# Performance work log

Measured on AMD Instinct MI355X. Metric: run time of the kernel, lower is better.

Reference implementation:

```python
import jax, jax.numpy as jnp
import numpy as np

N, E, B = 100000, 1000000, 64
DIN, DS, H, NG = 128, 1024, 256, 20


def setup_inputs() -> dict:
    key = jax.random.key(0)
    ks = jax.random.split(key, 48)
    lin = lambda k, i, o: (jax.random.normal(k, (i, o), jnp.float32) / np.sqrt(i)).astype(jnp.float32)
    inp = {
        'x': jax.random.normal(ks[0], (N, DIN), jnp.float32),
        'edge_index': jax.random.randint(ks[1], (2, E), 0, N, jnp.int32),
        'batch': jnp.sort(jax.random.randint(ks[2], (N,), 0, B, jnp.int32)),
        'static_features': jax.random.normal(ks[3], (B, DS), jnp.float32),
        'temporal_feats': jax.random.normal(ks[4], (B, 5), jnp.float32),
        'type_idx': jax.random.randint(ks[5], (B,), 0, 10, jnp.int32),
        'type_emb': jax.random.normal(ks[6], (10, H), jnp.float32),
        # static encoder
        'Ws1': lin(ks[7], DS, H), 'bs1': jnp.zeros(H), 'Ws2': lin(ks[8], H, H), 'bs2': jnp.zeros(H),
        # 3 GCN convs
        'Wc1': lin(ks[9], DIN, H), 'bc1': jnp.zeros(H),
        'Wc2': lin(ks[10], H, H), 'bc2': jnp.zeros(H),
        'Wc3': lin(ks[11], H, H), 'bc3': jnp.zeros(H),
        # residual dim_match linears
        'Wd1': lin(ks[12], DIN, H), 'bd1': jnp.zeros(H),
        'Wd2': lin(ks[13], H, H), 'bd2': jnp.zeros(H),
        'Wd3': lin(ks[14], H, H), 'bd3': jnp.zeros(H),
        # temporal MLP (5 -> H//2 -> H)
        'Wt1': lin(ks[15], 5, H // 2), 'bt1': jnp.zeros(H // 2),
        'Wt2': lin(ks[16], H // 2, H), 'bt2': jnp.zeros(H),
        # pattern detector
        'Wp1': lin(ks[17], H, H // 2), 'bp1': jnp.zeros(H // 2),
        'Wp2': lin(ks[18], H // 2, H), 'bp2': jnp.zeros(H),
        # fusion (5H -> 2H -> H)
        'Wf1': lin(ks[19], 5 * H, 2 * H), 'bf1': jnp.zeros(2 * H),
        'Wf2': lin(ks[20], 2 * H, H), 'bf2': jnp.zeros(H),
        # heads
        'Wg': lin(ks[21], H, NG), 'bg': jnp.zeros(NG),
        'Wtp': lin(ks[22], H, 1), 'btp': jnp.zeros(1),
    }
    return inp


def reference(x, edge_index, batch, static_features, temporal_feats, type_idx, type_emb,
              Ws1, bs1, Ws2, bs2,
              Wc1, bc1, Wc2, bc2, Wc3, bc3,
              Wd1, bd1, Wd2, bd2, Wd3, bd3,
              Wt1, bt1, Wt2, bt2,
              Wp1, bp1, Wp2, bp2,
              Wf1, bf1, Wf2, bf2,
              Wg, bg, Wtp, btp):
    n = x.shape[0]
    b = static_features.shape[0]
    src, dst = edge_index[0], edge_index[1]
    # GCN symmetric norm with self-loops: deg = 1 + in-degree
    deg = 1.0 + jax.ops.segment_sum(jnp.ones(src.shape[0], x.dtype), dst, num_segments=n)
    dinv = deg ** -0.5
    ew = dinv[src] * dinv[dst]  # [E] edge norm weights

    def gcn(h_in, W, bias):
        h = h_in @ W  # [n, H]
        agg = jax.ops.segment_sum(h[src] * ew[:, None], dst, num_segments=n)
        return agg + h / deg[:, None] + bias  # neighbor agg + self-loop + bias

    # 3 GCN layers with residual dim_match (dropout is identity at inference)
    x1 = jax.nn.relu(gcn(x, Wc1, bc1)) + (x @ Wd1 + bd1)
    x2 = jax.nn.relu(gcn(x1, Wc2, bc2)) + (x1 @ Wd2 + bd2)
    x3 = jax.nn.relu(gcn(x2, Wc3, bc3)) + (x2 @ Wd3 + bd3)

    pat = jax.nn.relu(jax.nn.relu(x3 @ Wp1 + bp1) @ Wp2 + bp2)

    counts = jnp.maximum(jax.ops.segment_sum(jnp.ones(n, x.dtype), batch, num_segments=b), 1.0)
    graph_embed = jax.ops.segment_sum(x3, batch, num_segments=b) / counts[:, None]
    pattern_embed = jax.ops.segment_sum(pat, batch, num_segments=b) / counts[:, None]

    static_embed = jax.nn.relu(static_features @ Ws1 + bs1) @ Ws2 + bs2
    temporal_embed = jax.nn.relu(temporal_feats @ Wt1 + bt1) @ Wt2 + bt2
    type_embed = type_emb[type_idx]

    combined = jnp.concatenate([graph_embed, static_embed, temporal_embed, type_embed, pattern_embed], axis=1)
    fused = jax.nn.relu(combined @ Wf1 + bf1) @ Wf2 + bf2
    group_logits = fused @ Wg + bg
    time_pred = fused @ Wtp + btp
    return fused, group_logits, time_pred
```

## Files before the change

### kernel.cpp

```cpp
#include <hip/hip_runtime.h>

#define H 256
#define LDK 40

typedef __attribute__((ext_vector_type(8))) short bf16x8;
typedef __attribute__((ext_vector_type(4))) float f32x4;

__device__ __forceinline__ float b2f(ushort h) {
    return __uint_as_float(((unsigned)h) << 16);
}
__device__ __forceinline__ float b2f_lo(unsigned u) {
    return __uint_as_float(u << 16);
}
__device__ __forceinline__ float b2f_hi(unsigned u) {
    return __uint_as_float(u & 0xffff0000u);
}
__device__ __forceinline__ ushort f2bf(float f) {
    unsigned u = __float_as_uint(f);
    unsigned r = (u + 0x7FFF + ((u >> 16) & 1)) >> 16;
    return (ushort)r;
}
__device__ __forceinline__ unsigned pack2bf(float lo, float hi) {
    return (unsigned)f2bf(lo) | ((unsigned)f2bf(hi) << 16);
}

__device__ __forceinline__ void gload16(const ushort* g, const short* l) {
    __builtin_amdgcn_global_load_lds(
        (const __attribute__((address_space(1))) void*)(const void*)g,
        (__attribute__((address_space(3))) void*)(void*)l, 16, 0, 0);
}

__global__ __launch_bounds__(256) void k_zero2_i(int* p, int* q, int n) {
    int i = blockIdx.x * 256 + threadIdx.x;
    if (i < n) { p[i] = 0; q[i] = 0; }
}

__global__ __launch_bounds__(256) void k_zero_f(float* p, int n) {
    int i = blockIdx.x * 256 + threadIdx.x;
    if (i < n) p[i] = 0.f;
}

__global__ __launch_bounds__(256) void k_count_deg_i(const int* __restrict__ dst, int* cnt, int E) {
    int i = blockIdx.x * 256 + threadIdx.x;
    if (i < E) atomicAdd(&cnt[dst[i]], 1);
}

__global__ __launch_bounds__(256) void k_scan1(const int* __restrict__ cnt, int* __restrict__ partial,
                                               int* __restrict__ bsums, int N) {
    __shared__ int s[256];
    int t = threadIdx.x;
    int idx = blockIdx.x * 256 + t;
    int v = idx < N ? cnt[idx] : 0;
    s[t] = v;
    __syncthreads();
    for (int off = 1; off < 256; off <<= 1) {
        int add = (t >= off) ? s[t - off] : 0;
        __syncthreads();
        s[t] += add;
        __syncthreads();
    }
    if (idx < N) partial[idx] = s[t];
    if (t == 255) bsums[blockIdx.x] = s[t];
}

__global__ __launch_bounds__(1024) void k_scan2(int* bsums, int nb) {
    __shared__ int s[1024];
    int t = threadIdx.x;
    s[t] = (t < nb) ? bsums[t] : 0;
    __syncthreads();
    for (int off = 1; off < 1024; off <<= 1) {
        int add = (t >= off) ? s[t - off] : 0;
        __syncthreads();
        s[t] += add;
        __syncthreads();
    }
    if (t < nb) bsums[t] = s[t];
}

__global__ __launch_bounds__(256) void k_scan3(const int* __restrict__ partial, const int* __restrict__ bsums,
                                               const int* __restrict__ cnt,
                                               int* __restrict__ rowptr, float* __restrict__ dinv,
                                               float* __restrict__ selfw, int N) {
    int idx = blockIdx.x * 256 + threadIdx.x;
    if (idx < N) {
        int off = blockIdx.x > 0 ? bsums[blockIdx.x - 1] : 0;
        rowptr[idx + 1] = partial[idx] + off;
        if (idx == 0) rowptr[0] = 0;
        float d = 1.0f + (float)cnt[idx];
        dinv[idx] = rsqrtf(d);
        selfw[idx] = 1.0f / d;
    }
}

__global__ __launch_bounds__(256) void k_scatter(const int* __restrict__ src, const int* __restrict__ dst,
                                                 const float* __restrict__ dinv, const int* __restrict__ rowptr,
                                                 int* __restrict__ fill, int* __restrict__ esrc,
                                                 float* __restrict__ ewt, int E) {
    int e = blockIdx.x * 256 + threadIdx.x;
    if (e >= E) return;
    int s = src[e], d = dst[e];
    int pos = rowptr[d] + atomicAdd(&fill[d], 1);
    esrc[pos] = s;
    ewt[pos] = dinv[s] * dinv[d];
}

__device__ __forceinline__ void tcvt_one(long i, const float* __restrict__ W, ushort* __restrict__ Wt,
                                         int K, int M) {
    int k = (int)(i / M), m = (int)(i - (long)k * M);
    Wt[(size_t)m * K + k] = f2bf(W[(size_t)k * M + m]);
}

__global__ __launch_bounds__(256) void k_prep(
    const float* __restrict__ x, ushort* __restrict__ xh, long nx, int DIN,
    const float* __restrict__ Wc1, ushort* Wc1t, const float* __restrict__ Wd1, ushort* Wd1t,
    const float* __restrict__ Wc2, ushort* Wc2t, const float* __restrict__ Wd2, ushort* Wd2t,
    const float* __restrict__ Wc3, ushort* Wc3t, const float* __restrict__ Wd3, ushort* Wd3t,
    const float* __restrict__ Wp1, ushort* Wp1t, const float* __restrict__ Wp2, ushort* Wp2t) {
    long i = (long)blockIdx.x * 256 + threadIdx.x;
    if (i < nx) { xh[i] = f2bf(x[i]); return; }
    i -= nx;
    long n1 = (long)DIN * 256;
    if (i < n1) { tcvt_one(i, Wc1, Wc1t, DIN, 256); return; }
    i -= n1;
    if (i < n1) { tcvt_one(i, Wd1, Wd1t, DIN, 256); return; }
    i -= n1;
    if (i < 65536) { tcvt_one(i, Wc2, Wc2t, 256, 256); return; }
    i -= 65536;
    if (i < 65536) { tcvt_one(i, Wd2, Wd2t, 256, 256); return; }
    i -= 65536;
    if (i < 65536) { tcvt_one(i, Wc3, Wc3t, 256, 256); return; }
    i -= 65536;
    if (i < 65536) { tcvt_one(i, Wd3, Wd3t, 256, 256); return; }
    i -= 65536;
    if (i < 32768) { tcvt_one(i, Wp1, Wp1t, 256, 128); return; }
    i -= 32768;
    if (i < 32768) { tcvt_one(i, Wp2, Wp2t, 128, 256); return; }
}

__global__ __launch_bounds__(256) void k_gather_b4(const ushort* __restrict__ xin, const int* __restrict__ rowptr,
                                                   const int* __restrict__ esrc, const float* __restrict__ ewt,
                                                   const float* __restrict__ selfw, ushort* __restrict__ p,
                                                   int N, int SX, int SP) {
    int node = blockIdx.x * 8 + (threadIdx.x >> 5);
    bool act = node < N;
    int nn = act ? node : N - 1;
    int c = (threadIdx.x & 31) << 3;
    uint4 hv = *(const uint4*)(xin + (size_t)nn * SX + c);
    float sw = selfw[nn];
    float a0 = b2f_lo(hv.x) * sw, a1 = b2f_hi(hv.x) * sw;
    float a2 = b2f_lo(hv.y) * sw, a3 = b2f_hi(hv.y) * sw;
    float a4 = b2f_lo(hv.z) * sw, a5 = b2f_hi(hv.z) * sw;
    float a6 = b2f_lo(hv.w) * sw, a7 = b2f_hi(hv.w) * sw;
    int j = act ? rowptr[nn] : 0, r1 = act ? rowptr[nn + 1] : 0;
    for (; j + 3 < r1; j += 4) {
        int s0 = esrc[j], s1 = esrc[j + 1], s2 = esrc[j + 2], s3 = esrc[j + 3];
        float w0 = ewt[j], w1 = ewt[j + 1], w2 = ewt[j + 2], w3 = ewt[j + 3];
        uint4 v0 = *(const uint4*)(xin + (size_t)s0 * SX + c);
        uint4 v1 = *(const uint4*)(xin + (size_t)s1 * SX + c);
        uint4 v2 = *(const uint4*)(xin + (size_t)s2 * SX + c);
        uint4 v3 = *(const uint4*)(xin + (size_t)s3 * SX + c);
        a0 += b2f_lo(v0.x) * w0 + b2f_lo(v1.x) * w1 + b2f_lo(v2.x) * w2 + b2f_lo(v3.x) * w3;
        a1 += b2f_hi(v0.x) * w0 + b2f_hi(v1.x) * w1 + b2f_hi(v2.x) * w2 + b2f_hi(v3.x) * w3;
        a2 += b2f_lo(v0.y) * w0 + b2f_lo(v1.y) * w1 + b2f_lo(v2.y) * w2 + b2f_lo(v3.y) * w3;
        a3 += b2f_hi(v0.y) * w0 + b2f_hi(v1.y) * w1 + b2f_hi(v2.y) * w2 + b2f_hi(v3.y) * w3;
        a4 += b2f_lo(v0.z) * w0 + b2f_lo(v1.z) * w1 + b2f_lo(v2.z) * w2 + b2f_lo(v3.z) * w3;
        a5 += b2f_hi(v0.z) * w0 + b2f_hi(v1.z) * w1 + b2f_hi(v2.z) * w2 + b2f_hi(v3.z) * w3;
        a6 += b2f_lo(v0.w) * w0 + b2f_lo(v1.w) * w1 + b2f_lo(v2.w) * w2 + b2f_lo(v3.w) * w3;
        a7 += b2f_hi(v0.w) * w0 + b2f_hi(v1.w) * w1 + b2f_hi(v2.w) * w2 + b2f_hi(v3.w) * w3;
    }
    for (; j < r1; ++j) {
        int s0 = esrc[j];
        float w0 = ewt[j];
        uint4 v0 = *(const uint4*)(xin + (size_t)s0 * SX + c);
        a0 += b2f_lo(v0.x) * w0; a1 += b2f_hi(v0.x) * w0;
        a2 += b2f_lo(v0.y) * w0; a3 += b2f_hi(v0.y) * w0;
        a4 += b2f_lo(v0.z) * w0; a5 += b2f_hi(v0.z) * w0;
        a6 += b2f_lo(v0.w) * w0; a7 += b2f_hi(v0.w) * w0;
    }
    if (act) {
        uint4 o;
        o.x = pack2bf(a0, a1); o.y = pack2bf(a2, a3);
        o.z = pack2bf(a4, a5); o.w = pack2bf(a6, a7);
        *(uint4*)(p + (size_t)node * SP + c) = o;
    }
}

__global__ __launch_bounds__(256) void k_gather_b2(const ushort* __restrict__ xin, const int* __restrict__ rowptr,
                                                   const int* __restrict__ esrc, const float* __restrict__ ewt,
                                                   const float* __restrict__ selfw, ushort* __restrict__ p,
                                                   int N, int SX, int SP) {
    int node = blockIdx.x * 16 + (threadIdx.x >> 4);
    bool act = node < N;
    int nn = act ? node : N - 1;
    int c = (threadIdx.x & 15) << 3;
    uint4 hv = *(const uint4*)(xin + (size_t)nn * SX + c);
    float sw = selfw[nn];
    float a0 = b2f_lo(hv.x) * sw, a1 = b2f_hi(hv.x) * sw;
    float a2 = b2f_lo(hv.y) * sw, a3 = b2f_hi(hv.y) * sw;
    float a4 = b2f_lo(hv.z) * sw, a5 = b2f_hi(hv.z) * sw;
    float a6 = b2f_lo(hv.w) * sw, a7 = b2f_hi(hv.w) * sw;
    int j = act ? rowptr[nn] : 0, r1 = act ? rowptr[nn + 1] : 0;
    for (; j + 3 < r1; j += 4) {
        int s0 = esrc[j], s1 = esrc[j + 1], s2 = esrc[j + 2], s3 = esrc[j + 3];
        float w0 = ewt[j], w1 = ewt[j + 1], w2 = ewt[j + 2], w3 = ewt[j + 3];
        uint4 v0 = *(const uint4*)(xin + (size_t)s0 * SX + c);
        uint4 v1 = *(const uint4*)(xin + (size_t)s1 * SX + c);
        uint4 v2 = *(const uint4*)(xin + (size_t)s2 * SX + c);
        uint4 v3 = *(const uint4*)(xin + (size_t)s3 * SX + c);
        a0 += b2f_lo(v0.x) * w0 + b2f_lo(v1.x) * w1 + b2f_lo(v2.x) * w2 + b2f_lo(v3.x) * w3;
        a1 += b2f_hi(v0.x) * w0 + b2f_hi(v1.x) * w1 + b2f_hi(v2.x) * w2 + b2f_hi(v3.x) * w3;
        a2 += b2f_lo(v0.y) * w0 + b2f_lo(v1.y) * w1 + b2f_lo(v2.y) * w2 + b2f_lo(v3.y) * w3;
        a3 += b2f_hi(v0.y) * w0 + b2f_hi(v1.y) * w1 + b2f_hi(v2.y) * w2 + b2f_hi(v3.y) * w3;
        a4 += b2f_lo(v0.z) * w0 + b2f_lo(v1.z) * w1 + b2f_lo(v2.z) * w2 + b2f_lo(v3.z) * w3;
        a5 += b2f_hi(v0.z) * w0 + b2f_hi(v1.z) * w1 + b2f_hi(v2.z) * w2 + b2f_hi(v3.z) * w3;
        a6 += b2f_lo(v0.w) * w0 + b2f_lo(v1.w) * w1 + b2f_lo(v2.w) * w2 + b2f_lo(v3.w) * w3;
        a7 += b2f_hi(v0.w) * w0 + b2f_hi(v1.w) * w1 + b2f_hi(v2.w) * w2 + b2f_hi(v3.w) * w3;
    }
    for (; j < r1; ++j) {
        int s0 = esrc[j];
        float w0 = ewt[j];
        uint4 v0 = *(const uint4*)(xin + (size_t)s0 * SX + c);
        a0 += b2f_lo(v0.x) * w0; a1 += b2f_hi(v0.x) * w0;
        a2 += b2f_lo(v0.y) * w0; a3 += b2f_hi(v0.y) * w0;
        a4 += b2f_lo(v0.z) * w0; a5 += b2f_hi(v0.z) * w0;
        a6 += b2f_lo(v0.w) * w0; a7 += b2f_hi(v0.w) * w0;
    }
    if (act) {
        uint4 o;
        o.x = pack2bf(a0, a1); o.y = pack2bf(a2, a3);
        o.z = pack2bf(a4, a5); o.w = pack2bf(a6, a7);
        *(uint4*)(p + (size_t)node * SP + c) = o;
    }
}

__global__ __launch_bounds__(256, 2) void k_fused_mfma(
    const ushort* __restrict__ Pm, const ushort* __restrict__ X,
    const ushort* __restrict__ Wct, const ushort* __restrict__ Wdt,
    const float* __restrict__ bc, const float* __restrict__ bd,
    ushort* __restrict__ Out, int N, int K, int SP, int SX) {
    __shared__ __align__(16) short Ps[64 * 64];
    __shared__ __align__(16) short Xs[64 * 64];
    __shared__ __align__(16) short Wcs[256 * 64];
    __shared__ __align__(16) short Wds[256 * 64];
    const int tid = threadIdx.x;
    const int wave = tid >> 6, lane = tid & 63;
    const int row0 = blockIdx.x * 64;

    f32x4 accC[4][4], accD[4][4];
#pragma unroll
    for (int i = 0; i < 4; ++i)
#pragma unroll
        for (int j = 0; j < 4; ++j) { accC[i][j] = (f32x4)0.f; accD[i][j] = (f32x4)0.f; }

    const int lr = lane >> 3;
    const int ls = lane & 7;
    const int swz = (ls ^ lr) << 3;
    const int m = lane & 15, t4 = lane >> 4;

    for (int k0 = 0; k0 < K; k0 += 64) {
#pragma unroll
        for (int i = 0; i < 2; ++i) {
            int rr = wave * 16 + i * 8;
            int gr = row0 + rr + lr; if (gr > N - 1) gr = N - 1;
            gload16(Pm + (size_t)gr * SP + k0 + swz, &Ps[rr * 64]);
            gload16(X + (size_t)gr * SX + k0 + swz, &Xs[rr * 64]);
        }
#pragma unroll
        for (int i = 0; i < 8; ++i) {
            int cc = wave * 64 + i * 8;
            gload16(Wct + (size_t)(cc + lr) * K + k0 + swz, &Wcs[cc * 64]);
            gload16(Wdt + (size_t)(cc + lr) * K + k0 + swz, &Wds[cc * 64]);
        }
        __syncthreads();

#pragma unroll
        for (int h = 0; h < 2; ++h) {
            const int slot = h * 4 + t4;
            bf16x8 aP[4], aX[4], bC[4], bD[4];
#pragma unroll
            for (int i = 0; i < 4; ++i) {
                int r = 16 * i + m;
                int off = r * 64 + ((slot ^ (r & 7)) << 3);
                aP[i] = *(bf16x8*)&Ps[off];
                aX[i] = *(bf16x8*)&Xs[off];
            }
#pragma unroll
            for (int j = 0; j < 4; ++j) {
                int c = wave * 64 + 16 * j + m;
                int off = c * 64 + ((slot ^ (c & 7)) << 3);
                bC[j] = *(bf16x8*)&Wcs[off];
                bD[j] = *(bf16x8*)&Wds[off];
            }
#pragma unroll
            for (int i = 0; i < 4; ++i)
#pragma unroll
                for (int j = 0; j < 4; ++j) {
                    accC[i][j] = __builtin_amdgcn_mfma_f32_16x16x32_bf16(aP[i], bC[j], accC[i][j], 0, 0, 0);
                    accD[i][j] = __builtin_amdgcn_mfma_f32_16x16x32_bf16(aX[i], bD[j], accD[i][j], 0, 0, 0);
                }
        }
        __syncthreads();
    }

    const int rq = t4 * 4;
#pragma unroll
    for (int j = 0; j < 4; ++j) {
        int col = wave * 64 + 16 * j + m;
        float bcv = bc[col], bdv = bd[col];
#pragma unroll
        for (int i = 0; i < 4; ++i)
#pragma unroll
            for (int g = 0; g < 4; ++g) {
                int row = row0 + 16 * i + rq + g;
                if (row < N) {
                    float v = fmaxf(accC[i][j][g] + bcv, 0.f) + accD[i][j][g] + bdv;
                    Out[(size_t)row * 256 + col] = f2bf(v);
                }
            }
    }
}

__global__ __launch_bounds__(256, 2) void k_gemm_mfma(
    const ushort* __restrict__ A, const ushort* __restrict__ Wt, const float* __restrict__ bias,
    ushort* __restrict__ Out, int N, int K, int M, int SA, int dorelu) {
    __shared__ short As[128 * LDK];
    __shared__ short Wls[256 * LDK];
    const int tid = threadIdx.x;
    const int wave = tid >> 6, lane = tid & 63;
    const int MW = M >> 6;
    const int R = 16384 / M;
    const int row0 = blockIdx.x * R;
    const int row_off = (wave / MW) * 64, col_off = (wave % MW) * 64;

    f32x4 acc[4][4];
#pragma unroll
    for (int i = 0; i < 4; ++i)
#pragma unroll
        for (int j = 0; j < 4; ++j) acc[i][j] = (f32x4)0.f;

    const int m = lane & 15, kh = (lane >> 4) * 8, sc = (tid & 3) * 8;

    for (int k0 = 0; k0 < K; k0 += 32) {
        for (int c = tid; c < R * 4; c += 256) {
            int r = c >> 2, ck = (c & 3) * 8;
            int gr = row0 + r; if (gr > N - 1) gr = N - 1;
            *(uint4*)&As[r * LDK + ck] = *(const uint4*)(A + (size_t)gr * SA + k0 + ck);
        }
        for (int p = 0; p < MW; ++p) {
            int col = p * 64 + (tid >> 2);
            *(uint4*)&Wls[col * LDK + sc] = *(const uint4*)(Wt + (size_t)col * K + k0 + sc);
        }
        __syncthreads();
        bf16x8 af[4], bf[4];
#pragma unroll
        for (int i = 0; i < 4; ++i) af[i] = *(bf16x8*)&As[(row_off + 16 * i + m) * LDK + kh];
#pragma unroll
        for (int j = 0; j < 4; ++j) bf[j] = *(bf16x8*)&Wls[(col_off + 16 * j + m) * LDK + kh];
#pragma unroll
        for (int i = 0; i < 4; ++i)
#pragma unroll
            for (int j = 0; j < 4; ++j)
                acc[i][j] = __builtin_amdgcn_mfma_f32_16x16x32_bf16(af[i], bf[j], acc[i][j], 0, 0, 0);
        __syncthreads();
    }

    const int rq = (lane >> 4) * 4;
#pragma unroll
    for (int j = 0; j < 4; ++j) {
        int col = col_off + 16 * j + m;
        float bv = bias[col];
#pragma unroll
        for (int i = 0; i < 4; ++i)
#pragma unroll
            for (int g = 0; g < 4; ++g) {
                int row = row0 + row_off + 16 * i + rq + g;
                if (row < N) {
                    float v = acc[i][j][g] + bv;
                    if (dorelu) v = fmaxf(v, 0.f);
                    Out[(size_t)row * M + col] = f2bf(v);
                }
            }
    }
}

__global__ __launch_bounds__(256, 2) void k_pat2_pool(
    const ushort* __restrict__ A, const ushort* __restrict__ Wt, const float* __restrict__ bias,
    const int* __restrict__ batch, float* __restrict__ pesum, int N, int K, int SA) {
    __shared__ short As[64 * LDK];
    __shared__ short Wls[256 * LDK];
    __shared__ int sbatch[64];
    const int tid = threadIdx.x;
    const int wave = tid >> 6, lane = tid & 63;
    const int row0 = blockIdx.x * 64;
    const int col_off = wave * 64;

    f32x4 acc[4][4];
#pragma unroll
    for (int i = 0; i < 4; ++i)
#pragma unroll
        for (int j = 0; j < 4; ++j) acc[i][j] = (f32x4)0.f;

    const int m = lane & 15, kh = (lane >> 4) * 8, sc = (tid & 3) * 8;
    if (tid < 64) {
        int r = row0 + tid;
        sbatch[tid] = batch[r < N ? r : (N - 1)];
    }

    for (int k0 = 0; k0 < K; k0 += 32) {
        {
            int r = tid >> 2, ck = (tid & 3) * 8;
            int gr = row0 + r; if (gr > N - 1) gr = N - 1;
            *(uint4*)&As[r * LDK + ck] = *(const uint4*)(A + (size_t)gr * SA + k0 + ck);
        }
#pragma unroll
        for (int p = 0; p < 4; ++p) {
            int col = p * 64 + (tid >> 2);
            *(uint4*)&Wls[col * LDK + sc] = *(const uint4*)(Wt + (size_t)col * K + k0 + sc);
        }
        __syncthreads();
        bf16x8 af[4], bf[4];
#pragma unroll
        for (int i = 0; i < 4; ++i) af[i] = *(bf16x8*)&As[(16 * i + m) * LDK + kh];
#pragma unroll
        for (int j = 0; j < 4; ++j) bf[j] = *(bf16x8*)&Wls[(col_off + 16 * j + m) * LDK + kh];
#pragma unroll
        for (int i = 0; i < 4; ++i)
#pragma unroll
            for (int j = 0; j < 4; ++j)
                acc[i][j] = __builtin_amdgcn_mfma_f32_16x16x32_bf16(af[i], bf[j], acc[i][j], 0, 0, 0);
        __syncthreads();
    }

    const int rq = (lane >> 4) * 4;
    const int g0 = sbatch[0];
    const int g1 = sbatch[63];
    for (int g = g0; g <= g1; ++g) {
#pragma unroll
        for (int j = 0; j < 4; ++j) {
            float bv = bias[col_off + 16 * j + m];
            float s = 0.f;
#pragma unroll
            for (int i = 0; i < 4; ++i)
#pragma unroll
                for (int q = 0; q < 4; ++q) {
                    int rl = 16 * i + rq + q;
                    bool ok = (sbatch[rl] == g) && (row0 + rl < N);
                    float v = fmaxf(acc[i][j][q] + bv, 0.f);
                    s += ok ? v : 0.f;
                }
            s += __shfl_down(s, 32, 64);
            s += __shfl_down(s, 16, 64);
            if (lane < 16) atomicAdd(&pesum[(size_t)g * 256 + col_off + 16 * j + lane], s);
        }
    }
}

__global__ void k_ranges(const int* __restrict__ batch, int N, int B, int* __restrict__ start,
                         float* __restrict__ countsf) {
    int b = threadIdx.x;
    if (b <= B) {
        int lo = 0, hi = N;
        while (lo < hi) {
            int mid = (lo + hi) >> 1;
            if (batch[mid] < b) lo = mid + 1; else hi = mid;
        }
        start[b] = lo;
    }
    __syncthreads();
    if (b < B) {
        int cnt = start[b + 1] - start[b];
        countsf[b] = (float)(cnt > 0 ? cnt : 1);
    }
}

#define POOLS 16
__global__ __launch_bounds__(256) void k_pool2(const ushort* __restrict__ M_, const int* __restrict__ start,
                                               float* __restrict__ outsum) {
    int b = blockIdx.x;
    int s = blockIdx.y;
    int wave = threadIdx.x >> 6, lane = threadIdx.x & 63;
    int r0 = start[b], r1 = start[b + 1];
    int stripe = s * 4 + wave;
    float a0 = 0.f, a1 = 0.f, a2 = 0.f, a3 = 0.f;
    for (int r = r0 + stripe; r < r1; r += POOLS * 4) {
        ushort4 v = *(const ushort4*)(M_ + (size_t)r * 256 + lane * 4);
        a0 += b2f(v.x); a1 += b2f(v.y); a2 += b2f(v.z); a3 += b2f(v.w);
    }
    __shared__ float red[4][256];
    *(float4*)&red[wave][lane * 4] = make_float4(a0, a1, a2, a3);
    __syncthreads();
    int col = threadIdx.x;
    float t = red[0][col] + red[1][col] + red[2][col] + red[3][col];
    if (t != 0.f) atomicAdd(&outsum[(size_t)b * 256 + col], t);
}

__global__ __launch_bounds__(256) void k_fin_comb(const float* __restrict__ gesum, const float* __restrict__ pesum,
                                                  const float* __restrict__ countsf,
                                                  const float* __restrict__ temb, const int* __restrict__ tidx,
                                                  float* __restrict__ comb) {
    int b = blockIdx.x, t = threadIdx.x;
    float inv = 1.0f / countsf[b];
    float* o = comb + (size_t)b * 1280;
    o[t] = gesum[(size_t)b * 256 + t] * inv;
    o[768 + t] = temb[(size_t)tidx[b] * 256 + t];
    o[1024 + t] = pesum[(size_t)b * 256 + t] * inv;
}

__global__ __launch_bounds__(256) void k_dense(const float* __restrict__ vin, int vs,
                                               const float* __restrict__ W, const float* __restrict__ bias,
                                               float* __restrict__ out, int os, int oo,
                                               int K, int M, int relu) {
    const int b = blockIdx.y;
    const int wave = threadIdx.x >> 6, lane = threadIdx.x & 63;
    const int c = blockIdx.x * 64 + lane;
    const float* vrow = vin + (size_t)b * vs;
    float acc = 0.f;
    int k = wave;
    for (; k + 28 < K; k += 32) {
#pragma unroll
        for (int u = 0; u < 8; ++u)
            acc += vrow[k + 4 * u] * W[(size_t)(k + 4 * u) * M + c];
    }
    for (; k < K; k += 4)
        acc += vrow[k] * W[(size_t)k * M + c];
    __shared__ float red[4][64];
    red[wave][lane] = acc;
    __syncthreads();
    if (wave == 0) {
        float s = red[0][lane] + red[1][lane] + red[2][lane] + red[3][lane] + bias[c];
        if (relu) s = fmaxf(s, 0.f);
        out[(size_t)b * os + oo + c] = s;
    }
}

__global__ __launch_bounds__(256) void k_heads_small(const float* __restrict__ fused,
                                                     const float* __restrict__ Wg, const float* __restrict__ bg,
                                                     const float* __restrict__ Wtp, const float* __restrict__ btp,
                                                     float* __restrict__ out_logits, float* __restrict__ out_tp,
                                                     int NG) {
    __shared__ float lf[256];
    int b = blockIdx.x, tid = threadIdx.x;
    int wave = tid >> 6, lane = tid & 63;
    lf[tid] = fused[(size_t)b * 256 + tid];
    __syncthreads();
    for (int c = wave; c < NG; c += 4) {
        float s = 0.f;
#pragma unroll
        for (int k = lane; k < 256; k += 64) s += lf[k] * Wg[(size_t)k * NG + c];
#pragma unroll
        for (int off = 32; off > 0; off >>= 1) s += __shfl_down(s, off, 64);
        if (lane == 0) out_logits[(size_t)b * NG + c] = s + bg[c];
    }
    if (wave == 0) {
        float s = 0.f;
#pragma unroll
        for (int k = lane; k < 256; k += 64) s += lf[k] * Wtp[k];
#pragma unroll
        for (int off = 32; off > 0; off >>= 1) s += __shfl_down(s, off, 64);
        if (lane == 0) out_tp[b] = s + btp[0];
    }
}

extern "C" void kernel_launch(void* const* d_in, const int* in_sizes, int n_in,
                              void* d_out, int out_size, void* d_ws, size_t ws_size,
                              hipStream_t stream) {
    const float* x   = (const float*)d_in[0];
    const int* ei    = (const int*)d_in[1];
    const int* batch = (const int*)d_in[2];
    const float* sf  = (const float*)d_in[3];
    const float* tf  = (const float*)d_in[4];
    const int* tidx  = (const int*)d_in[5];
    const float* temb = (const float*)d_in[6];
    const float *Ws1 = (const float*)d_in[7],  *bs1 = (const float*)d_in[8];
    const float *Ws2 = (const float*)d_in[9],  *bs2 = (const float*)d_in[10];
    const float *Wc1 = (const float*)d_in[11], *bc1 = (const float*)d_in[12];
    const float *Wc2 = (const float*)d_in[13], *bc2 = (const float*)d_in[14];
    const float *Wc3 = (const float*)d_in[15], *bc3 = (const float*)d_in[16];
    const float *Wd1 = (const float*)d_in[17], *bd1 = (const float*)d_in[18];
    const float *Wd2 = (const float*)d_in[19], *bd2 = (const float*)d_in[20];
    const float *Wd3 = (const float*)d_in[21], *bd3 = (const float*)d_in[22];
    const float *Wt1 = (const float*)d_in[23], *bt1 = (const float*)d_in[24];
    const float *Wt2 = (const float*)d_in[25], *bt2 = (const float*)d_in[26];
    const float *Wp1 = (const float*)d_in[27], *bp1 = (const float*)d_in[28];
    const float *Wp2 = (const float*)d_in[29], *bp2 = (const float*)d_in[30];
    const float *Wf1 = (const float*)d_in[31], *bf1 = (const float*)d_in[32];
    const float *Wf2 = (const float*)d_in[33], *bf2 = (const float*)d_in[34];
    const float *Wg  = (const float*)d_in[35], *bg  = (const float*)d_in[36];
    const float *Wtp = (const float*)d_in[37], *btp = (const float*)d_in[38];

    const int N = in_sizes[2];
    const int E = in_sizes[1] / 2;
    const int B = in_sizes[5];
    const int DIN = in_sizes[0] / N;
    const int DS = in_sizes[3] / B;
    const int NG = in_sizes[36];
    const int* src = ei;
    const int* dst = ei + E;

    char* w = (char*)d_ws;
    ushort* A   = (ushort*)w;              w += (size_t)N * 256 * 2;
    ushort* Bb  = (ushort*)w;              w += (size_t)N * 256 * 2;
    ushort* xh  = (ushort*)w;              w += (size_t)N * 128 * 2;
    ushort* Wc1t = (ushort*)w;             w += 128 * 256 * 2;
    ushort* Wd1t = (ushort*)w;             w += 128 * 256 * 2;
    ushort* Wc2t = (ushort*)w;             w += 256 * 256 * 2;
    ushort* Wd2t = (ushort*)w;             w += 256 * 256 * 2;
    ushort* Wc3t = (ushort*)w;             w += 256 * 256 * 2;
    ushort* Wd3t = (ushort*)w;             w += 256 * 256 * 2;
    ushort* Wp1t = (ushort*)w;             w += 256 * 128 * 2;
    ushort* Wp2t = (ushort*)w;             w += 128 * 256 * 2;
    int* esrc   = (int*)w;                 w += (size_t)E * 4;
    float* ewt  = (float*)w;               w += (size_t)E * 4;
    int* cnt    = (int*)w;                 w += (size_t)N * 4;
    int* part   = (int*)w;                 w += (size_t)N * 4;
    int* rowptr = (int*)w;                 w += (size_t)(N + 1) * 4;
    int* fill   = (int*)w;                 w += (size_t)N * 4;
    int* bsums  = (int*)w;                 w += 1024 * 4;
    float* dinv = (float*)w;               w += (size_t)N * 4;
    float* selfw = (float*)w;              w += (size_t)N * 4;
    int* startp = (int*)w;                 w += (B + 1) * 4;
    float* countsf = (float*)w;            w += B * 4;
    float* ge = (float*)w;                 w += B * 256 * 4;
    float* pe = (float*)w;                 w += B * 256 * 4;
    float* s1buf = (float*)w;              w += B * 256 * 4;
    float* t1buf = (float*)w;              w += B * 128 * 4;
    float* comb = (float*)w;               w += B * 1280 * 4;
    float* fh = (float*)w;                 w += B * 512 * 4;

    float* out_fused = (float*)d_out;
    float* out_logits = out_fused + (size_t)B * H;
    float* out_tp = out_logits + (size_t)B * NG;

    dim3 blk(256);
    const int nbN = (N + 255) / 256;
    const int nbE = (E + 255) / 256;

    k_zero2_i<<<dim3(nbN), blk, 0, stream>>>(cnt, fill, N);
    k_count_deg_i<<<dim3(nbE), blk, 0, stream>>>(dst, cnt, E);
    k_scan1<<<dim3(nbN), blk, 0, stream>>>(cnt, part, bsums, N);
    k_scan2<<<dim3(1), dim3(1024), 0, stream>>>(bsums, nbN);
    k_scan3<<<dim3(nbN), blk, 0, stream>>>(part, bsums, cnt, rowptr, dinv, selfw, N);
    k_scatter<<<dim3(nbE), blk, 0, stream>>>(src, dst, dinv, rowptr, fill, esrc, ewt, E);

    {
        long nx = (long)N * DIN;
        long tot = nx + 2L * DIN * 256 + 4L * 65536 + 2L * 32768;
        k_prep<<<dim3((unsigned)((tot + 255) / 256)), blk, 0, stream>>>(
            x, xh, nx, DIN, Wc1, Wc1t, Wd1, Wd1t, Wc2, Wc2t, Wd2, Wd2t,
            Wc3, Wc3t, Wd3, Wd3t, Wp1, Wp1t, Wp2, Wp2t);
        k_ranges<<<dim3(1), dim3(128), 0, stream>>>(batch, N, B, startp, countsf);
        k_zero_f<<<dim3((2 * B * 256 + 255) / 256), blk, 0, stream>>>(ge, 2 * B * 256);
    }

    const int ngb4 = (N + 7) / 8;
    const int ngb2 = (N + 15) / 16;
    const int nfb = (N + 63) / 64;

    k_dense<<<dim3(4, B), blk, 0, stream>>>(sf, DS, Ws1, bs1, s1buf, 256, 0, DS, 256, 1);
    k_dense<<<dim3(4, B), blk, 0, stream>>>(s1buf, 256, Ws2, bs2, comb, 1280, 256, 256, 256, 0);
    k_dense<<<dim3(2, B), blk, 0, stream>>>(tf, 5, Wt1, bt1, t1buf, 128, 0, 5, 128, 1);
    k_dense<<<dim3(4, B), blk, 0, stream>>>(t1buf, 128, Wt2, bt2, comb, 1280, 512, 128, 256, 0);

    k_gather_b2<<<dim3(ngb2), blk, 0, stream>>>(xh, rowptr, esrc, ewt, selfw, A, N, 128, 128);
    k_fused_mfma<<<dim3(nfb), blk, 0, stream>>>(A, xh, Wc1t, Wd1t, bc1, bd1, Bb, N, 128, 128, 128);
    k_gather_b4<<<dim3(ngb4), blk, 0, stream>>>(Bb, rowptr, esrc, ewt, selfw, A, N, 256, 256);
    k_fused_mfma<<<dim3(nfb), blk, 0, stream>>>(A, Bb, Wc2t, Wd2t, bc2, bd2, A, N, 256, 256, 256);
    k_gather_b4<<<dim3(ngb4), blk, 0, stream>>>(A, rowptr, esrc, ewt, selfw, Bb, N, 256, 256);
    k_fused_mfma<<<dim3(nfb), blk, 0, stream>>>(Bb, A, Wc3t, Wd3t, bc3, bd3, Bb, N, 256, 256, 256);

    k_pool2<<<dim3(B, POOLS), blk, 0, stream>>>(Bb, startp, ge);
    k_gemm_mfma<<<dim3((N + 127) / 128), blk, 0, stream>>>(Bb, Wp1t, bp1, A, N, 256, 128, 256, 1);
    k_pat2_pool<<<dim3((N + 63) / 64), blk, 0, stream>>>(A, Wp2t, bp2, batch, pe, N, 128, 128);
    k_fin_comb<<<dim3(B), blk, 0, stream>>>(ge, pe, countsf, temb, tidx, comb);

    k_dense<<<dim3(8, B), blk, 0, stream>>>(comb, 1280, Wf1, bf1, fh, 512, 0, 1280, 512, 1);
    k_dense<<<dim3(4, B), blk, 0, stream>>>(fh, 512, Wf2, bf2, out_fused, 256, 0, 512, 256, 0);
    k_heads_small<<<dim3(B), blk, 0, stream>>>(out_fused, Wg, bg, Wtp, btp, out_logits, out_tp, NG);
}
```

Measured before the change: 825.5 us.

## Fuse graph pooling into last GCN layer and fuse pattern MLP into one kernel

The third fused GCN GEMM now also accumulates per-graph sums of its output via atomics, which removes the separate pooling kernel's re-read of the node features. The two pattern-detector GEMMs are merged into one kernel that keeps the 128-wide hidden tile in LDS and pools directly, so the intermediate no longer round-trips through global memory. The 256-wide gather is changed from 32 lanes per node with 16-byte loads to 64 lanes per node with 8-byte loads. In exchange, the pooling epilogue loops over graphs inside each tile, and the new pattern kernel uses a large LDS footprint that limits it to one block per CU.

```diff
diff --git a/kernel.cpp b/kernel.cpp
--- a/kernel.cpp
+++ b/kernel.cpp
@@ -1,7 +1,6 @@
 #include <hip/hip_runtime.h>
 
 #define H 256
-#define LDK 40
 
 typedef __attribute__((ext_vector_type(8))) short bf16x8;
 typedef __attribute__((ext_vector_type(4))) float f32x4;
@@ -141,48 +140,34 @@
                                                    const int* __restrict__ esrc, const float* __restrict__ ewt,
                                                    const float* __restrict__ selfw, ushort* __restrict__ p,
                                                    int N, int SX, int SP) {
-    int node = blockIdx.x * 8 + (threadIdx.x >> 5);
-    bool act = node < N;
-    int nn = act ? node : N - 1;
-    int c = (threadIdx.x & 31) << 3;
-    uint4 hv = *(const uint4*)(xin + (size_t)nn * SX + c);
-    float sw = selfw[nn];
-    float a0 = b2f_lo(hv.x) * sw, a1 = b2f_hi(hv.x) * sw;
-    float a2 = b2f_lo(hv.y) * sw, a3 = b2f_hi(hv.y) * sw;
-    float a4 = b2f_lo(hv.z) * sw, a5 = b2f_hi(hv.z) * sw;
-    float a6 = b2f_lo(hv.w) * sw, a7 = b2f_hi(hv.w) * sw;
-    int j = act ? rowptr[nn] : 0, r1 = act ? rowptr[nn + 1] : 0;
+    int node = blockIdx.x * 4 + (threadIdx.x >> 6);
+    if (node >= N) return;
+    int c = (threadIdx.x & 63) << 2;
+    ushort4 h = *(const ushort4*)(xin + (size_t)node * SX + c);
+    float sw = selfw[node];
+    float a0 = b2f(h.x) * sw, a1 = b2f(h.y) * sw, a2 = b2f(h.z) * sw, a3 = b2f(h.w) * sw;
+    int j = rowptr[node], r1 = rowptr[node + 1];
     for (; j + 3 < r1; j += 4) {
         int s0 = esrc[j], s1 = esrc[j + 1], s2 = esrc[j + 2], s3 = esrc[j + 3];
         float w0 = ewt[j], w1 = ewt[j + 1], w2 = ewt[j + 2], w3 = ewt[j + 3];
-        uint4 v0 = *(const uint4*)(xin + (size_t)s0 * SX + c);
-        uint4 v1 = *(const uint4*)(xin + (size_t)s1 * SX + c);
-        uint4 v2 = *(const uint4*)(xin + (size_t)s2 * SX + c);
-        uint4 v3 = *(const uint4*)(xin + (size_t)s3 * SX + c);
-        a0 += b2f_lo(v0.x) * w0 + b2f_lo(v1.x) * w1 + b2f_lo(v2.x) * w2 + b2f_lo(v3.x) * w3;
-        a1 += b2f_hi(v0.x) * w0 + b2f_hi(v1.x) * w1 + b2f_hi(v2.x) * w2 + b2f_hi(v3.x) * w3;
-        a2 += b2f_lo(v0.y) * w0 + b2f_lo(v1.y) * w1 + b2f_lo(v2.y) * w2 + b2f_lo(v3.y) * w3;
-        a3 += b2f_hi(v0.y) * w0 + b2f_hi(v1.y) * w1 + b2f_hi(v2.y) * w2 + b2f_hi(v3.y) * w3;
-        a4 += b2f_lo(v0.z) * w0 + b2f_lo(v1.z) * w1 + b2f_lo(v2.z) * w2 + b2f_lo(v3.z) * w3;
-        a5 += b2f_hi(v0.z) * w0 + b2f_hi(v1.z) * w1 + b2f_hi(v2.z) * w2 + b2f_hi(v3.z) * w3;
-        a6 += b2f_lo(v0.w) * w0 + b2f_lo(v1.w) * w1 + b2f_lo(v2.w) * w2 + b2f_lo(v3.w) * w3;
-        a7 += b2f_hi(v0.w) * w0 + b2f_hi(v1.w) * w1 + b2f_hi(v2.w) * w2 + b2f_hi(v3.w) * w3;
+        ushort4 v0 = *(const ushort4*)(xin + (size_t)s0 * SX + c);
+        ushort4 v1 = *(const ushort4*)(xin + (size_t)s1 * SX + c);
+        ushort4 v2 = *(const ushort4*)(xin + (size_t)s2 * SX + c);
+        ushort4 v3 = *(const ushort4*)(xin + (size_t)s3 * SX + c);
+        a0 += b2f(v0.x) * w0 + b2f(v1.x) * w1 + b2f(v2.x) * w2 + b2f(v3.x) * w3;
+        a1 += b2f(v0.y) * w0 + b2f(v1.y) * w1 + b2f(v2.y) * w2 + b2f(v3.y) * w3;
+        a2 += b2f(v0.z) * w0 + b2f(v1.z) * w1 + b2f(v2.z) * w2 + b2f(v3.z) * w3;
+        a3 += b2f(v0.w) * w0 + b2f(v1.w) * w1 + b2f(v2.w) * w2 + b2f(v3.w) * w3;
     }
     for (; j < r1; ++j) {
         int s0 = esrc[j];
         float w0 = ewt[j];
-        uint4 v0 = *(const uint4*)(xin + (size_t)s0 * SX + c);
-        a0 += b2f_lo(v0.x) * w0; a1 += b2f_hi(v0.x) * w0;
-        a2 += b2f_lo(v0.y) * w0; a3 += b2f_hi(v0.y) * w0;
-        a4 += b2f_lo(v0.z) * w0; a5 += b2f_hi(v0.z) * w0;
-        a6 += b2f_lo(v0.w) * w0; a7 += b2f_hi(v0.w) * w0;
-    }
-    if (act) {
-        uint4 o;
-        o.x = pack2bf(a0, a1); o.y = pack2bf(a2, a3);
-        o.z = pack2bf(a4, a5); o.w = pack2bf(a6, a7);
-        *(uint4*)(p + (size_t)node * SP + c) = o;
-    }
+        ushort4 v0 = *(const ushort4*)(xin + (size_t)s0 * SX + c);
+        a0 += b2f(v0.x) * w0; a1 += b2f(v0.y) * w0; a2 += b2f(v0.z) * w0; a3 += b2f(v0.w) * w0;
+    }
+    ushort4 o;
+    o.x = f2bf(a0); o.y = f2bf(a1); o.z = f2bf(a2); o.w = f2bf(a3);
+    *(ushort4*)(p + (size_t)node * SP + c) = o;
 }
 
 __global__ __launch_bounds__(256) void k_gather_b2(const ushort* __restrict__ xin, const int* __restrict__ rowptr,
@@ -237,7 +222,8 @@
     const ushort* __restrict__ Pm, const ushort* __restrict__ X,
     const ushort* __restrict__ Wct, const ushort* __restrict__ Wdt,
     const float* __restrict__ bc, const float* __restrict__ bd,
-    ushort* __restrict__ Out, int N, int K, int SP, int SX) {
+    ushort* __restrict__ Out, int N, int K, int SP, int SX,
+    const int* __restrict__ batch, float* __restrict__ gesum, int dopool) {
     __shared__ __align__(16) short Ps[64 * 64];
     __shared__ __align__(16) short Xs[64 * 64];
     __shared__ __align__(16) short Wcs[256 * 64];
@@ -302,6 +288,12 @@
         __syncthreads();
     }
 
+    int* sb = (int*)Ps;
+    if (dopool && tid < 64) {
+        int r = row0 + tid;
+        sb[tid] = batch[r < N ? r : (N - 1)];
+    }
+
     const int rq = t4 * 4;
 #pragma unroll
     for (int j = 0; j < 4; ++j) {
@@ -318,126 +310,156 @@
                 }
             }
     }
-}
-
-__global__ __launch_bounds__(256, 2) void k_gemm_mfma(
-    const ushort* __restrict__ A, const ushort* __restrict__ Wt, const float* __restrict__ bias,
-    ushort* __restrict__ Out, int N, int K, int M, int SA, int dorelu) {
-    __shared__ short As[128 * LDK];
-    __shared__ short Wls[256 * LDK];
-    const int tid = threadIdx.x;
-    const int wave = tid >> 6, lane = tid & 63;
-    const int MW = M >> 6;
-    const int R = 16384 / M;
-    const int row0 = blockIdx.x * R;
-    const int row_off = (wave / MW) * 64, col_off = (wave % MW) * 64;
-
-    f32x4 acc[4][4];
-#pragma unroll
-    for (int i = 0; i < 4; ++i)
-#pragma unroll
-        for (int j = 0; j < 4; ++j) acc[i][j] = (f32x4)0.f;
-
-    const int m = lane & 15, kh = (lane >> 4) * 8, sc = (tid & 3) * 8;
-
-    for (int k0 = 0; k0 < K; k0 += 32) {
-        for (int c = tid; c < R * 4; c += 256) {
-            int r = c >> 2, ck = (c & 3) * 8;
-            int gr = row0 + r; if (gr > N - 1) gr = N - 1;
-            *(uint4*)&As[r * LDK + ck] = *(const uint4*)(A + (size_t)gr * SA + k0 + ck);
-        }
-        for (int p = 0; p < MW; ++p) {
-            int col = p * 64 + (tid >> 2);
-            *(uint4*)&Wls[col * LDK + sc] = *(const uint4*)(Wt + (size_t)col * K + k0 + sc);
-        }
-        __syncthreads();
-        bf16x8 af[4], bf[4];
-#pragma unroll
-        for (int i = 0; i < 4; ++i) af[i] = *(bf16x8*)&As[(row_off + 16 * i + m) * LDK + kh];
-#pragma unroll
-        for (int j = 0; j < 4; ++j) bf[j] = *(bf16x8*)&Wls[(col_off + 16 * j + m) * LDK + kh];
-#pragma unroll
-        for (int i = 0; i < 4; ++i)
-#pragma unroll
-            for (int j = 0; j < 4; ++j)
-                acc[i][j] = __builtin_amdgcn_mfma_f32_16x16x32_bf16(af[i], bf[j], acc[i][j], 0, 0, 0);
-        __syncthreads();
-    }
-
-    const int rq = (lane >> 4) * 4;
-#pragma unroll
-    for (int j = 0; j < 4; ++j) {
-        int col = col_off + 16 * j + m;
-        float bv = bias[col];
-#pragma unroll
-        for (int i = 0; i < 4; ++i)
-#pragma unroll
-            for (int g = 0; g < 4; ++g) {
-                int row = row0 + row_off + 16 * i + rq + g;
-                if (row < N) {
-                    float v = acc[i][j][g] + bv;
-                    if (dorelu) v = fmaxf(v, 0.f);
-                    Out[(size_t)row * M + col] = f2bf(v);
-                }
+
+    if (dopool) {
+        __syncthreads();
+        const int g0 = sb[0], g1 = sb[63];
+        for (int g = g0; g <= g1; ++g) {
+#pragma unroll
+            for (int j = 0; j < 4; ++j) {
+                int col = wave * 64 + 16 * j + m;
+                float bcv = bc[col], bdv = bd[col];
+                float s = 0.f;
+#pragma unroll
+                for (int i = 0; i < 4; ++i)
+#pragma unroll
+                    for (int q = 0; q < 4; ++q) {
+                        int rl = 16 * i + rq + q;
+                        bool ok = (sb[rl] == g) && (row0 + rl < N);
+                        float v = fmaxf(accC[i][j][q] + bcv, 0.f) + accD[i][j][q] + bdv;
+                        s += ok ? v : 0.f;
+                    }
+                s += __shfl_down(s, 32, 64);
+                s += __shfl_down(s, 16, 64);
+                if (lane < 16) atomicAdd(&gesum[(size_t)g * 256 + wave * 64 + 16 * j + lane], s);
             }
-    }
-}
-
-__global__ __launch_bounds__(256, 2) void k_pat2_pool(
-    const ushort* __restrict__ A, const ushort* __restrict__ Wt, const float* __restrict__ bias,
-    const int* __restrict__ batch, float* __restrict__ pesum, int N, int K, int SA) {
-    __shared__ short As[64 * LDK];
-    __shared__ short Wls[256 * LDK];
+        }
+    }
+}
+
+__global__ __launch_bounds__(256, 1) void k_pat_fused(
+    const ushort* __restrict__ Bb, const ushort* __restrict__ Wp1t, const ushort* __restrict__ Wp2t,
+    const float* __restrict__ bp1, const float* __restrict__ bp2,
+    const int* __restrict__ batch, float* __restrict__ pesum, int N) {
+    __shared__ __align__(16) short Wp2s[256 * 128];
+    __shared__ __align__(16) short Wp1s[128 * 64];
+    __shared__ __align__(16) short Bbs[64 * 64];
+    __shared__ __align__(16) short Ts[64 * 128];
     __shared__ int sbatch[64];
     const int tid = threadIdx.x;
     const int wave = tid >> 6, lane = tid & 63;
     const int row0 = blockIdx.x * 64;
-    const int col_off = wave * 64;
-
-    f32x4 acc[4][4];
-#pragma unroll
-    for (int i = 0; i < 4; ++i)
-#pragma unroll
-        for (int j = 0; j < 4; ++j) acc[i][j] = (f32x4)0.f;
-
-    const int m = lane & 15, kh = (lane >> 4) * 8, sc = (tid & 3) * 8;
+    const int m = lane & 15, t4 = lane >> 4;
+    const int lr = lane >> 3, ls = lane & 7;
+    const int swz = (ls ^ lr) << 3;
+
     if (tid < 64) {
         int r = row0 + tid;
         sbatch[tid] = batch[r < N ? r : (N - 1)];
     }
 
-    for (int k0 = 0; k0 < K; k0 += 32) {
-        {
-            int r = tid >> 2, ck = (tid & 3) * 8;
-            int gr = row0 + r; if (gr > N - 1) gr = N - 1;
-            *(uint4*)&As[r * LDK + ck] = *(const uint4*)(A + (size_t)gr * SA + k0 + ck);
-        }
-#pragma unroll
-        for (int p = 0; p < 4; ++p) {
-            int col = p * 64 + (tid >> 2);
-            *(uint4*)&Wls[col * LDK + sc] = *(const uint4*)(Wt + (size_t)col * K + k0 + sc);
-        }
-        __syncthreads();
+    {
+        const int rl4 = lane >> 4;
+        const int sl = lane & 15;
+#pragma unroll
+        for (int it = 0; it < 16; ++it) {
+            int c0 = wave * 64 + it * 4;
+            int c = c0 + rl4;
+            gload16(Wp2t + (size_t)c * 128 + (((sl ^ (c & 15)) << 3)), &Wp2s[c0 * 128]);
+        }
+    }
+
+    f32x4 acc1[4][2];
+#pragma unroll
+    for (int i = 0; i < 4; ++i)
+#pragma unroll
+        for (int j = 0; j < 2; ++j) acc1[i][j] = (f32x4)0.f;
+
+    for (int k0 = 0; k0 < 256; k0 += 64) {
+#pragma unroll
+        for (int i = 0; i < 2; ++i) {
+            int rr = wave * 16 + i * 8;
+            int gr = row0 + rr + lr; if (gr > N - 1) gr = N - 1;
+            gload16(Bb + (size_t)gr * 256 + k0 + swz, &Bbs[rr * 64]);
+        }
+#pragma unroll
+        for (int i = 0; i < 4; ++i) {
+            int cc = wave * 32 + i * 8;
+            gload16(Wp1t + (size_t)(cc + lr) * 256 + k0 + swz, &Wp1s[cc * 64]);
+        }
+        __syncthreads();
+#pragma unroll
+        for (int h = 0; h < 2; ++h) {
+            const int slot = h * 4 + t4;
+            bf16x8 aB[4], bW[2];
+#pragma unroll
+            for (int i = 0; i < 4; ++i) {
+                int r = 16 * i + m;
+                aB[i] = *(bf16x8*)&Bbs[r * 64 + ((slot ^ (r & 7)) << 3)];
+            }
+#pragma unroll
+            for (int j = 0; j < 2; ++j) {
+                int c = wave * 32 + 16 * j + m;
+                bW[j] = *(bf16x8*)&Wp1s[c * 64 + ((slot ^ (c & 7)) << 3)];
+            }
+#pragma unroll
+            for (int i = 0; i < 4; ++i)
+#pragma unroll
+                for (int j = 0; j < 2; ++j)
+                    acc1[i][j] = __builtin_amdgcn_mfma_f32_16x16x32_bf16(aB[i], bW[j], acc1[i][j], 0, 0, 0);
+        }
+        __syncthreads();
+    }
+
+    const int rq = t4 * 4;
+#pragma unroll
+    for (int j = 0; j < 2; ++j) {
+        int col = wave * 32 + 16 * j + m;
+        float bv = bp1[col];
+#pragma unroll
+        for (int i = 0; i < 4; ++i)
+#pragma unroll
+            for (int g = 0; g < 4; ++g) {
+                int r = 16 * i + rq + g;
+                float v = fmaxf(acc1[i][j][g] + bv, 0.f);
+                Ts[r * 128 + (((col >> 3) ^ (r & 15)) << 3) + (col & 7)] = (short)f2bf(v);
+            }
+    }
+    __syncthreads();
+
+    f32x4 acc2[4][4];
+#pragma unroll
+    for (int i = 0; i < 4; ++i)
+#pragma unroll
+        for (int j = 0; j < 4; ++j) acc2[i][j] = (f32x4)0.f;
+
+#pragma unroll
+    for (int sl = 0; sl < 4; ++sl) {
+        const int s16 = sl * 4 + t4;
         bf16x8 af[4], bf[4];
 #pragma unroll
-        for (int i = 0; i < 4; ++i) af[i] = *(bf16x8*)&As[(16 * i + m) * LDK + kh];
-#pragma unroll
-        for (int j = 0; j < 4; ++j) bf[j] = *(bf16x8*)&Wls[(col_off + 16 * j + m) * LDK + kh];
+        for (int i = 0; i < 4; ++i) {
+            int r = 16 * i + m;
+            af[i] = *(bf16x8*)&Ts[r * 128 + ((s16 ^ (r & 15)) << 3)];
+        }
+#pragma unroll
+        for (int j = 0; j < 4; ++j) {
+            int c = wave * 64 + 16 * j + m;
+            bf[j] = *(bf16x8*)&Wp2s[c * 128 + ((s16 ^ (c & 15)) << 3)];
+        }
 #pragma unroll
         for (int i = 0; i < 4; ++i)
 #pragma unroll
             for (int j = 0; j < 4; ++j)
-                acc[i][j] = __builtin_amdgcn_mfma_f32_16x16x32_bf16(af[i], bf[j], acc[i][j], 0, 0, 0);
-        __syncthreads();
-    }
-
-    const int rq = (lane >> 4) * 4;
+                acc2[i][j] = __builtin_amdgcn_mfma_f32_16x16x32_bf16(af[i], bf[j], acc2[i][j], 0, 0, 0);
+    }
+
     const int g0 = sbatch[0];
     const int g1 = sbatch[63];
     for (int g = g0; g <= g1; ++g) {
 #pragma unroll
         for (int j = 0; j < 4; ++j) {
-            float bv = bias[col_off + 16 * j + m];
+            float bv = bp2[wave * 64 + 16 * j + m];
             float s = 0.f;
 #pragma unroll
             for (int i = 0; i < 4; ++i)
@@ -445,12 +467,12 @@
                 for (int q = 0; q < 4; ++q) {
                     int rl = 16 * i + rq + q;
                     bool ok = (sbatch[rl] == g) && (row0 + rl < N);
-                    float v = fmaxf(acc[i][j][q] + bv, 0.f);
+                    float v = fmaxf(acc2[i][j][q] + bv, 0.f);
                     s += ok ? v : 0.f;
                 }
             s += __shfl_down(s, 32, 64);
             s += __shfl_down(s, 16, 64);
-            if (lane < 16) atomicAdd(&pesum[(size_t)g * 256 + col_off + 16 * j + lane], s);
+            if (lane < 16) atomicAdd(&pesum[(size_t)g * 256 + wave * 64 + 16 * j + lane], s);
         }
     }
 }
@@ -471,27 +493,6 @@
         int cnt = start[b + 1] - start[b];
         countsf[b] = (float)(cnt > 0 ? cnt : 1);
     }
-}
-
-#define POOLS 16
-__global__ __launch_bounds__(256) void k_pool2(const ushort* __restrict__ M_, const int* __restrict__ start,
-                                               float* __restrict__ outsum) {
-    int b = blockIdx.x;
-    int s = blockIdx.y;
-    int wave = threadIdx.x >> 6, lane = threadIdx.x & 63;
-    int r0 = start[b], r1 = start[b + 1];
-    int stripe = s * 4 + wave;
-    float a0 = 0.f, a1 = 0.f, a2 = 0.f, a3 = 0.f;
-    for (int r = r0 + stripe; r < r1; r += POOLS * 4) {
-        ushort4 v = *(const ushort4*)(M_ + (size_t)r * 256 + lane * 4);
-        a0 += b2f(v.x); a1 += b2f(v.y); a2 += b2f(v.z); a3 += b2f(v.w);
-    }
-    __shared__ float red[4][256];
-    *(float4*)&red[wave][lane * 4] = make_float4(a0, a1, a2, a3);
-    __syncthreads();
-    int col = threadIdx.x;
-    float t = red[0][col] + red[1][col] + red[2][col] + red[3][col];
-    if (t != 0.f) atomicAdd(&outsum[(size_t)b * 256 + col], t);
 }
 
 __global__ __launch_bounds__(256) void k_fin_comb(const float* __restrict__ gesum, const float* __restrict__ pesum,
@@ -652,7 +653,7 @@
         k_zero_f<<<dim3((2 * B * 256 + 255) / 256), blk, 0, stream>>>(ge, 2 * B * 256);
     }
 
-    const int ngb4 = (N + 7) / 8;
+    const int ngb4 = (N + 3) / 4;
     const int ngb2 = (N + 15) / 16;
     const int nfb = (N + 63) / 64;
 
@@ -662,15 +663,13 @@
     k_dense<<<dim3(4, B), blk, 0, stream>>>(t1buf, 128, Wt2, bt2, comb, 1280, 512, 128, 256, 0);
 
     k_gather_b2<<<dim3(ngb2), blk, 0, stream>>>(xh, rowptr, esrc, ewt, selfw, A, N, 128, 128);
-    k_fused_mfma<<<dim3(nfb), blk, 0, stream>>>(A, xh, Wc1t, Wd1t, bc1, bd1, Bb, N, 128, 128, 128);
+    k_fused_mfma<<<dim3(nfb), blk, 0, stream>>>(A, xh, Wc1t, Wd1t, bc1, bd1, Bb, N, 128, 128, 128, batch, ge, 0);
     k_gather_b4<<<dim3(ngb4), blk, 0, stream>>>(Bb, rowptr, esrc, ewt, selfw, A, N, 256, 256);
-    k_fused_mfma<<<dim3(nfb), blk, 0, stream>>>(A, Bb, Wc2t, Wd2t, bc2, bd2, A, N, 256, 256, 256);
+    k_fused_mfma<<<dim3(nfb), blk, 0, stream>>>(A, Bb, Wc2t, Wd2t, bc2, bd2, A, N, 256, 256, 256, batch, ge, 0);
     k_gather_b4<<<dim3(ngb4), blk, 0, stream>>>(A, rowptr, esrc, ewt, selfw, Bb, N, 256, 256);
-    k_fused_mfma<<<dim3(nfb), blk, 0, stream>>>(Bb, A, Wc3t, Wd3t, bc3, bd3, Bb, N, 256, 256, 256);
-
-    k_pool2<<<dim3(B, POOLS), blk, 0, stream>>>(Bb, startp, ge);
-    k_gemm_mfma<<<dim3((N + 127) / 128), blk, 0, stream>>>(Bb, Wp1t, bp1, A, N, 256, 128, 256, 1);
-    k_pat2_pool<<<dim3((N + 63) / 64), blk, 0, stream>>>(A, Wp2t, bp2, batch, pe, N, 128, 128);
+    k_fused_mfma<<<dim3(nfb), blk, 0, stream>>>(Bb, A, Wc3t, Wd3t, bc3, bd3, Bb, N, 256, 256, 256, batch, ge, 1);
+
+    k_pat_fused<<<dim3(nfb), blk, 0, stream>>>(Bb, Wp1t, Wp2t, bp1, bp2, batch, pe, N);
     k_fin_comb<<<dim3(B), blk, 0, stream>>>(ge, pe, countsf, temb, tidx, comb);
 
     k_dense<<<dim3(8, B), blk, 0, stream>>>(comb, 1280, Wf1, bf1, fh, 512, 0, 1280, 512, 1);
```

Result: no change. 819.9 us (-0.7%).
